# Optimization experiments

Measured on AMD Instinct MI355X. Metric: run time of the kernel, lower is better.

The kernel has to match this reference:

```python
import jax, jax.numpy as jnp
import numpy as np

B, S, D, H = 2, 1024, 1024, 16
HD = D // H
WINDOW = 256
FFN = 4 * D


def setup_inputs() -> dict:
    key = jax.random.key(0)
    ks = jax.random.split(key, 12)
    xav = lambda k, o, i: jax.random.normal(k, (o, i), jnp.float32) * np.sqrt(2.0 / (o + i))
    return {
        "x": jax.random.normal(ks[0], (B, S, D), jnp.float32),
        "wq": xav(ks[1], D, D), "bq": jnp.zeros((D,), jnp.float32),
        "wk": xav(ks[2], D, D), "bk": jnp.zeros((D,), jnp.float32),
        "wv": xav(ks[3], D, D), "bv": jnp.zeros((D,), jnp.float32),
        "wo": xav(ks[4], D, D), "bo": jnp.zeros((D,), jnp.float32),
        "attn_norm_w": jnp.ones((D,), jnp.float32),
        "ffn_norm_w": jnp.ones((D,), jnp.float32),
        "gate_w": xav(ks[5], FFN, D),
        "up_w": xav(ks[6], FFN, D),
        "down_w": xav(ks[7], D, FFN),
    }


def _rms(x, w):
    return x * jax.lax.rsqrt(jnp.mean(x * x, axis=-1, keepdims=True) + 1e-6) * w


def _rotate_half(x):
    x1, x2 = jnp.split(x, 2, axis=-1)
    return jnp.concatenate([-x2, x1], axis=-1)


def _rope_cos_sin(seq_len, head_dim):
    inv_freq = 1.0 / (10000.0 ** (jnp.arange(0, head_dim, 2, dtype=jnp.float32) / head_dim))
    freqs = jnp.arange(seq_len, dtype=jnp.float32)[:, None] * inv_freq[None, :]  # [S, HD/2]
    emb = jnp.concatenate([freqs, freqs], axis=-1)  # [S, HD]
    return jnp.cos(emb)[None, None], jnp.sin(emb)[None, None]  # [1,1,S,HD]


def reference(x, wq, bq, wk, bk, wv, bv, wo, bo, attn_norm_w, ffn_norm_w, gate_w, up_w, down_w):
    b, s, d = x.shape
    scale = 1.0 / np.sqrt(HD)
    residual = x
    h = _rms(x, attn_norm_w)
    q = (h @ wq.T + bq).reshape(b, s, H, HD).transpose(0, 2, 1, 3)  # [B,H,S,HD]
    k = (h @ wk.T + bk).reshape(b, s, H, HD).transpose(0, 2, 1, 3)
    v = (h @ wv.T + bv).reshape(b, s, H, HD).transpose(0, 2, 1, 3)
    cos, sin = _rope_cos_sin(s, HD)
    q = q * cos + _rotate_half(q) * sin
    k = k * cos + _rotate_half(k) * sin
    scores = jnp.einsum("bhqd,bhkd->bhqk", q, k) * scale  # dense [B,H,S,S]
    i = jnp.arange(s)[:, None]
    j = jnp.arange(s)[None, :]
    local_mask = (j <= i) & (i - j < WINDOW)  # causal sliding window
    scores = jnp.where(local_mask[None, None], scores, -jnp.inf)
    attn = jax.nn.softmax(scores, axis=-1)
    out = jnp.einsum("bhqk,bhkd->bhqd", attn, v)
    out = out.transpose(0, 2, 1, 3).reshape(b, s, d) @ wo.T + bo
    x = residual + out
    residual = x
    h = _rms(x, ffn_norm_w)
    ffn = (jax.nn.silu(h @ gate_w.T) * (h @ up_w.T)) @ down_w.T
    return (residual + ffn, attn)
```

## Files before the change

### kernel.cpp

```cpp
#include <hip/hip_runtime.h>

typedef unsigned short u16;
typedef unsigned int u32;
typedef __attribute__((ext_vector_type(8))) short short8;
typedef __attribute__((ext_vector_type(4))) float f32x4;

__device__ __forceinline__ float b2fu(u32 u) {
  union { u32 i; float f; } v; v.i = u << 16; return v.f;
}
__device__ __forceinline__ u16 f2bu(float f) {
  union { float f; u32 i; } v; v.f = f;
  u32 r = (v.i + 0x7fffu + ((v.i >> 16) & 1u)) >> 16;
  return (u16)r;
}
__device__ __forceinline__ void gl_lds16(const void* g, void* l) {
  __builtin_amdgcn_global_load_lds((const __attribute__((address_space(1))) void*)g,
                                   (__attribute__((address_space(3))) void*)l, 16, 0, 0);
}
__device__ __forceinline__ short8 ld_lds_b8(const u16* p) {
  uint2 a = *(const uint2*)p;
  uint2 b = *(const uint2*)(p + 4);
  union { u32 u[4]; short8 s; } v;
  v.u[0] = a.x; v.u[1] = a.y; v.u[2] = b.x; v.u[3] = b.y;
  return v.s;
}

__global__ __launch_bounds__(256) void cvt_front(
    const float* __restrict__ wq, const float* __restrict__ wk,
    const float* __restrict__ wv, const float* __restrict__ wo,
    const float* __restrict__ wg, const float* __restrict__ wu,
    const float* __restrict__ wd, u16* __restrict__ dst,
    const float* __restrict__ bq, const float* __restrict__ bk,
    const float* __restrict__ bv, float* __restrict__ bqkv,
    const float* __restrict__ x, const float* __restrict__ anw,
    u16* __restrict__ h1)
{
  __shared__ float red[4];
  if (blockIdx.x >= 16387) {
    const int row = blockIdx.x - 16387;
    const int t = threadIdx.x;
    float4 v = ((const float4*)(x + (size_t)row * 1024))[t];
    float ss = v.x * v.x + v.y * v.y + v.z * v.z + v.w * v.w;
#pragma unroll
    for (int m = 32; m > 0; m >>= 1) ss += __shfl_xor(ss, m, 64);
    if ((t & 63) == 0) red[t >> 6] = ss;
    __syncthreads();
    float tot = red[0] + red[1] + red[2] + red[3];
    float r = rsqrtf(tot * (1.0f / 1024.0f) + 1e-6f);
    float4 wv4 = ((const float4*)anw)[t];
    ushort4 o = make_ushort4(f2bu(v.x * r * wv4.x), f2bu(v.y * r * wv4.y),
                             f2bu(v.z * r * wv4.z), f2bu(v.w * r * wv4.w));
    ((ushort4*)(h1 + (size_t)row * 1024))[t] = o;
    return;
  }
  if (blockIdx.x >= 16384) {
    const int s = blockIdx.x - 16384;
    const float* bsrc = (s == 0) ? bq : (s == 1) ? bk : bv;
    const int o = threadIdx.x * 4;
    *(float4*)(bqkv + s * 1024 + o) = *(const float4*)(bsrc + o);
    return;
  }
  size_t e = ((size_t)blockIdx.x * 256 + threadIdx.x) * 4;
  size_t seg = e >> 20;
  const float* src; size_t soff;
  if      (seg == 0) { src = wq; soff = e; }
  else if (seg == 1) { src = wk; soff = e - ((size_t)1 << 20); }
  else if (seg == 2) { src = wv; soff = e - ((size_t)2 << 20); }
  else if (seg == 3) { src = wo; soff = e - ((size_t)3 << 20); }
  else if (seg < 12) {
    size_t idx = e - ((size_t)4 << 20);
    int rc = (int)(idx >> 10);
    int col = (int)(idx & 1023);
    int bi = rc >> 5, j = rc & 31;
    if (j < 16) { src = wg; soff = (size_t)(bi * 16 + j) * 1024 + col; }
    else        { src = wu; soff = (size_t)(bi * 16 + j - 16) * 1024 + col; }
  }
  else { src = wd; soff = e - ((size_t)12 << 20); }
  float4 v = *(const float4*)(src + soff);
  *(ushort4*)(dst + e) = make_ushort4(f2bu(v.x), f2bu(v.y), f2bu(v.z), f2bu(v.w));
}

__global__ __launch_bounds__(256) void rmsnorm_kernel(
    const float* __restrict__ x, const float* __restrict__ w, u16* __restrict__ out)
{
  const int row = blockIdx.x;
  const int t = threadIdx.x;
  float4 v = ((const float4*)(x + (size_t)row * 1024))[t];
  float ss = v.x * v.x + v.y * v.y + v.z * v.z + v.w * v.w;
#pragma unroll
  for (int m = 32; m > 0; m >>= 1) ss += __shfl_xor(ss, m, 64);
  __shared__ float red[4];
  if ((t & 63) == 0) red[t >> 6] = ss;
  __syncthreads();
  float tot = red[0] + red[1] + red[2] + red[3];
  float r = rsqrtf(tot * (1.0f / 1024.0f) + 1e-6f);
  float4 wv = ((const float4*)w)[t];
  ushort4 o = make_ushort4(f2bu(v.x * r * wv.x), f2bu(v.y * r * wv.y),
                           f2bu(v.z * r * wv.z), f2bu(v.w * r * wv.w));
  ((ushort4*)(out + (size_t)row * 1024))[t] = o;
}

template<int TMB, int TNB, int EPI, bool HAS_BIAS, bool HAS_RES, bool SPLIT>
__global__ __launch_bounds__(256) void gemm_bt(
    const u16* __restrict__ A, const u16* __restrict__ B, float* __restrict__ C,
    const float* __restrict__ bias, const float* __restrict__ res,
    int M, int N, int K, int lda,
    u16* __restrict__ P0, u16* __restrict__ P1, u16* __restrict__ P2)
{
  constexpr int BK = 32;
  constexpr int WTM = TMB / 2, WTN = TNB / 2;
  constexpr int MT = WTM / 16, NT = WTN / 16;
  __shared__ u16 As[TMB * BK];
  __shared__ u16 Bs[TNB * BK];
  const int t = threadIdx.x;
  const int w = t >> 6, l = t & 63;
  const int wm = (w >> 1) * WTM, wn = (w & 1) * WTN;
  const int lr = l & 15, lq = l >> 4;
  const int tile_m = blockIdx.y * TMB, tile_n = blockIdx.x * TNB;
  const int kb = SPLIT ? blockIdx.z * K : 0;
  if (SPLIT) C += (size_t)blockIdx.z * M * N;

  f32x4 acc[MT][NT] = {};

  const int sr = t >> 2;
  const int sc8 = (t & 3) * 8;
  const u16* Ab = A + (size_t)(tile_m + sr) * lda + kb + sc8;
  const u16* Bb = B + (size_t)(tile_n + sr) * lda + kb + sc8;

  for (int kk = 0; kk < K; kk += BK) {
#pragma unroll
    for (int i = 0; i < TMB / 64; ++i)
      gl_lds16(Ab + kk + (size_t)i * 64 * lda, &As[t * 8 + i * 2048]);
#pragma unroll
    for (int i = 0; i < TNB / 64; ++i)
      gl_lds16(Bb + kk + (size_t)i * 64 * lda, &Bs[t * 8 + i * 2048]);
    __syncthreads();
    short8 af[MT], bfr[NT];
#pragma unroll
    for (int mt = 0; mt < MT; ++mt)
      af[mt] = *(const short8*)&As[(wm + mt * 16 + lr) * BK + lq * 8];
#pragma unroll
    for (int nt = 0; nt < NT; ++nt)
      bfr[nt] = *(const short8*)&Bs[(wn + nt * 16 + lr) * BK + lq * 8];
#pragma unroll
    for (int mt = 0; mt < MT; ++mt)
#pragma unroll
      for (int nt = 0; nt < NT; ++nt)
        acc[mt][nt] = __builtin_amdgcn_mfma_f32_16x16x32_bf16(af[mt], bfr[nt], acc[mt][nt], 0, 0, 0);
    __syncthreads();
  }

  if (EPI == 0) {
#pragma unroll
    for (int nt = 0; nt < NT; ++nt) {
      const int col = tile_n + wn + nt * 16 + lr;
      const float bv = HAS_BIAS ? bias[col] : 0.0f;
#pragma unroll
      for (int mt = 0; mt < MT; ++mt) {
        const int row0 = tile_m + wm + mt * 16 + lq * 4;
#pragma unroll
        for (int r = 0; r < 4; ++r) {
          const size_t off = (size_t)(row0 + r) * N + col;
          float v = acc[mt][nt][r] + bv;
          if (HAS_RES) v += res[off];
          C[off] = v;
        }
      }
    }
  } else if (EPI == 1) {
    const int colbase = tile_n + wn;
    const int seg = colbase >> 10;
    const int h = (colbase >> 6) & 15;
    u16* dstb = (seg == 0) ? P0 : (seg == 1) ? P1 : P2;
    float bv[NT];
#pragma unroll
    for (int nt = 0; nt < NT; ++nt) bv[nt] = bias[colbase + nt * 16 + lr];
#pragma unroll
    for (int mt = 0; mt < MT; ++mt) {
      const int row0 = tile_m + wm + mt * 16 + lq * 4;
#pragma unroll
      for (int r = 0; r < 4; ++r) {
        const int row = row0 + r;
        const int s = row & 1023, b = row >> 10;
        u16* dst = dstb + (((size_t)(b * 16 + h) << 10) + s) * 64;
        if (seg < 2) {
#pragma unroll
          for (int np = 0; np < 2; ++np) {
            const int i = np * 16 + lr;
            const float th = (float)s * exp2f(-0.4152410118609203f * (float)i);
            float sn, cs; __sincosf(th, &sn, &cs);
            const float g0 = acc[mt][np][r] + bv[np];
            const float g2 = acc[mt][np + 2][r] + bv[np + 2];
            dst[i]      = f2bu(g0 * cs - g2 * sn);
            dst[i + 32] = f2bu(g2 * cs + g0 * sn);
          }
        } else {
#pragma unroll
          for (int nt = 0; nt < NT; ++nt)
            dst[nt * 16 + lr] = f2bu(acc[mt][nt][r] + bv[nt]);
        }
      }
    }
  } else {
#pragma unroll
    for (int nt = 0; nt < NT; nt += 2) {
      const int feat = (((tile_n + wn + nt * 16) >> 5) << 4) + lr;
#pragma unroll
      for (int mt = 0; mt < MT; ++mt) {
        const int row0 = tile_m + wm + mt * 16 + lq * 4;
#pragma unroll
        for (int r = 0; r < 4; ++r) {
          const float g = acc[mt][nt][r];
          const float u = acc[mt][nt + 1][r];
          const float a = g / (1.0f + __expf(-g)) * u;
          P0[(size_t)(row0 + r) * (N >> 1) + feat] = f2bu(a);
        }
      }
    }
  }
}

__global__ __launch_bounds__(256) void reduce2_kernel(
    const float* __restrict__ p, const float* __restrict__ bias,
    const float* __restrict__ res, float* __restrict__ out)
{
  const size_t i = ((size_t)blockIdx.x * 256 + threadIdx.x) * 4;
  float4 a = *(const float4*)(p + i);
  float4 b = *(const float4*)(p + i + 2097152);
  float4 r = *(const float4*)(res + i);
  float4 bv = *(const float4*)(bias + (i & 1023));
  float4 o;
  o.x = r.x + bv.x + a.x + b.x;
  o.y = r.y + bv.y + a.y + b.y;
  o.z = r.z + bv.z + a.z + b.z;
  o.w = r.w + bv.w + a.w + b.w;
  *(float4*)(out + i) = o;
}

__global__ __launch_bounds__(256) void reduce4_kernel(
    const float* __restrict__ p, const float* __restrict__ res, float* __restrict__ out)
{
  const size_t i = ((size_t)blockIdx.x * 256 + threadIdx.x) * 4;
  float4 a = *(const float4*)(p + i);
  float4 b = *(const float4*)(p + i + 2097152);
  float4 c = *(const float4*)(p + i + 2 * 2097152);
  float4 d = *(const float4*)(p + i + 3 * 2097152);
  float4 r = *(const float4*)(res + i);
  float4 o;
  o.x = r.x + a.x + b.x + c.x + d.x;
  o.y = r.y + a.y + b.y + c.y + d.y;
  o.z = r.z + a.z + b.z + c.z + d.z;
  o.w = r.w + a.w + b.w + c.w + d.w;
  *(float4*)(out + i) = o;
}

#define KP 68
#define PP 292

__global__ __launch_bounds__(256) void attn_kernel(
    const u16* __restrict__ qb, const u16* __restrict__ kb, const u16* __restrict__ vb,
    float* __restrict__ probs, u16* __restrict__ ctx)
{
  __shared__ u16 Kbuf[288 * KP];
  __shared__ u16 Vbuf[288 * KP];
  __shared__ float smax[2][32];
  __shared__ float ssum[2][32];
  u16* Pbuf = Kbuf;

  const int blk = blockIdx.x;
  const int qt = blk & 31, bh = blk >> 5;
  const int b = bh >> 4, h = bh & 15;
  const int q0 = qt << 5;
  const int kstart = (q0 > 255) ? (q0 - 255) : 0;
  const int span = q0 + 32 - kstart;
  const int t = threadIdx.x;
  const int w = t >> 6, l = t & 63;
  const int lr = l & 15, lq = l >> 4;
  const int mw = w & 1, nh = w >> 1;
  const size_t bhS = (size_t)bh << 10;

  {
    const u16* kg = kb + ((bhS + (size_t)kstart) << 6);
    const u16* vg = vb + ((bhS + (size_t)kstart) << 6);
    for (int idx = t; idx < 288 * 8; idx += 256) {
      const int r = idx >> 3, c = (idx & 7) << 3;
      uint4 kv4 = make_uint4(0, 0, 0, 0), vv4 = make_uint4(0, 0, 0, 0);
      if (r < span) {
        kv4 = *(const uint4*)&kg[(r << 6) + c];
        vv4 = *(const uint4*)&vg[(r << 6) + c];
      }
      *(uint2*)&Kbuf[r * KP + c]     = make_uint2(kv4.x, kv4.y);
      *(uint2*)&Kbuf[r * KP + c + 4] = make_uint2(kv4.z, kv4.w);
      *(uint2*)&Vbuf[r * KP + c]     = make_uint2(vv4.x, vv4.y);
      *(uint2*)&Vbuf[r * KP + c + 4] = make_uint2(vv4.z, vv4.w);
    }
  }
  short8 qa0, qa1;
  {
    const u16* qrow = qb + ((bhS + (size_t)(q0 + mw * 16 + lr)) << 6) + lq * 8;
    qa0 = *(const short8*)qrow;
    qa1 = *(const short8*)(qrow + 32);
  }
  __syncthreads();

  f32x4 acc[9];
#pragma unroll
  for (int i = 0; i < 9; ++i) acc[i] = (f32x4){0.f, 0.f, 0.f, 0.f};
#pragma unroll
  for (int i = 0; i < 9; ++i) {
    const int nt = nh + 2 * i;
    const u16* kr = &Kbuf[(nt * 16 + lr) * KP + lq * 8];
    short8 kf0 = ld_lds_b8(kr);
    short8 kf1 = ld_lds_b8(kr + 32);
    acc[i] = __builtin_amdgcn_mfma_f32_16x16x32_bf16(qa0, kf0, acc[i], 0, 0, 0);
    acc[i] = __builtin_amdgcn_mfma_f32_16x16x32_bf16(qa1, kf1, acc[i], 0, 0, 0);
  }

  const int rbase = mw * 16 + lq * 4;
  float rmax[4] = {-1e30f, -1e30f, -1e30f, -1e30f};
#pragma unroll
  for (int i = 0; i < 9; ++i) {
    const int jg = kstart + (nh + 2 * i) * 16 + lr;
#pragma unroll
    for (int r = 0; r < 4; ++r) {
      const int q = q0 + rbase + r;
      const bool valid = (jg >= q - 255) && (jg <= q);
      const float v = valid ? acc[i][r] * 0.125f : -1e30f;
      acc[i][r] = v;
      rmax[r] = fmaxf(rmax[r], v);
    }
  }
#pragma unroll
  for (int r = 0; r < 4; ++r) {
    float m_ = rmax[r];
    m_ = fmaxf(m_, __shfl_xor(m_, 1, 64));
    m_ = fmaxf(m_, __shfl_xor(m_, 2, 64));
    m_ = fmaxf(m_, __shfl_xor(m_, 4, 64));
    m_ = fmaxf(m_, __shfl_xor(m_, 8, 64));
    rmax[r] = m_;
  }
  if (lr == 0) {
#pragma unroll
    for (int r = 0; r < 4; ++r) smax[nh][rbase + r] = rmax[r];
  }
  __syncthreads();
#pragma unroll
  for (int r = 0; r < 4; ++r)
    rmax[r] = fmaxf(smax[0][rbase + r], smax[1][rbase + r]);
  float rsum[4] = {0.f, 0.f, 0.f, 0.f};
#pragma unroll
  for (int i = 0; i < 9; ++i)
#pragma unroll
    for (int r = 0; r < 4; ++r) {
      const float p = exp2f((acc[i][r] - rmax[r]) * 1.44269504f);
      acc[i][r] = p;
      rsum[r] += p;
    }
#pragma unroll
  for (int r = 0; r < 4; ++r) {
    float s_ = rsum[r];
    s_ += __shfl_xor(s_, 1, 64);
    s_ += __shfl_xor(s_, 2, 64);
    s_ += __shfl_xor(s_, 4, 64);
    s_ += __shfl_xor(s_, 8, 64);
    rsum[r] = s_;
  }
  if (lr == 0) {
#pragma unroll
    for (int r = 0; r < 4; ++r) ssum[nh][rbase + r] = rsum[r];
  }
  __syncthreads();

  float inv4[4];
#pragma unroll
  for (int r = 0; r < 4; ++r)
    inv4[r] = 1.0f / (ssum[0][rbase + r] + ssum[1][rbase + r]);
#pragma unroll
  for (int i = 0; i < 9; ++i) {
    const int nt = nh + 2 * i;
#pragma unroll
    for (int r = 0; r < 4; ++r)
      Pbuf[(rbase + r) * PP + nt * 16 + lr] = f2bu(acc[i][r] * inv4[r]);
  }
  __syncthreads();

  {
    const int row = t >> 3;
    const int q = q0 + row;
    const int c0 = (t & 7) << 7;
    const int lo = q - 255;
    float* prow = probs + ((bhS + (size_t)q) << 10) + c0;
    const u16* pr = &Pbuf[row * PP];
#pragma unroll 4
    for (int cc = 0; cc < 128; cc += 4) {
      const int c = c0 + cc;
      float4 o;
      o.x = (c + 0 >= lo && c + 0 <= q) ? b2fu(pr[c + 0 - kstart]) : 0.0f;
      o.y = (c + 1 >= lo && c + 1 <= q) ? b2fu(pr[c + 1 - kstart]) : 0.0f;
      o.z = (c + 2 >= lo && c + 2 <= q) ? b2fu(pr[c + 2 - kstart]) : 0.0f;
      o.w = (c + 3 >= lo && c + 3 <= q) ? b2fu(pr[c + 3 - kstart]) : 0.0f;
      *(float4*)&prow[cc] = o;
    }
  }

  const int n0 = (w >> 1) * 2;
  f32x4 oacc[2] = {};
#pragma unroll
  for (int ks = 0; ks < 9; ++ks) {
    short8 pa = ld_lds_b8(&Pbuf[(mw * 16 + lr) * PP + ks * 32 + lq * 8]);
#pragma unroll
    for (int nn = 0; nn < 2; ++nn) {
      const int d = (n0 + nn) * 16 + lr;
      union { u16 u[8]; short8 s; } bf_;
#pragma unroll
      for (int jj = 0; jj < 8; ++jj)
        bf_.u[jj] = Vbuf[(ks * 32 + lq * 8 + jj) * KP + d];
      oacc[nn] = __builtin_amdgcn_mfma_f32_16x16x32_bf16(pa, bf_.s, oacc[nn], 0, 0, 0);
    }
  }
#pragma unroll
  for (int nn = 0; nn < 2; ++nn) {
    const int d = (n0 + nn) * 16 + lr;
#pragma unroll
    for (int r = 0; r < 4; ++r) {
      const int q = q0 + rbase + r;
      ctx[(((size_t)(b * 1024 + q)) << 10) + (h << 6) + d] = f2bu(oacc[nn][r]);
    }
  }
}

extern "C" void kernel_launch(void* const* d_in, const int* in_sizes, int n_in,
                              void* d_out, int out_size, void* d_ws, size_t ws_size,
                              hipStream_t stream) {
  (void)in_sizes; (void)n_in; (void)out_size; (void)ws_size;
  const float* x   = (const float*)d_in[0];
  const float* wq  = (const float*)d_in[1];
  const float* bq  = (const float*)d_in[2];
  const float* wk  = (const float*)d_in[3];
  const float* bk  = (const float*)d_in[4];
  const float* wv  = (const float*)d_in[5];
  const float* bv  = (const float*)d_in[6];
  const float* wo  = (const float*)d_in[7];
  const float* bo  = (const float*)d_in[8];
  const float* anw = (const float*)d_in[9];
  const float* fnw = (const float*)d_in[10];
  const float* wg  = (const float*)d_in[11];
  const float* wu  = (const float*)d_in[12];
  const float* wd  = (const float*)d_in[13];

  char* ws = (char*)d_ws;
  u16*   wbf  = (u16*)ws;
  float* bqkv = (float*)(ws + ((size_t)32 << 20));
  u16*   h1   = (u16*)(ws + ((size_t)32 << 20) + (16 << 10));
  char*  R    = ws + ((size_t)36 << 20) + (16 << 10);
  u16*   qbp  = (u16*)R;
  u16*   kbp  = (u16*)(R + ((size_t)4 << 20));
  u16*   vbp  = (u16*)(R + ((size_t)8 << 20));
  u16*   ctx  = (u16*)(R + ((size_t)12 << 20));
  float* x1   = (float*)(R + ((size_t)16 << 20));
  u16*   h2   = (u16*)(R + ((size_t)24 << 20));
  u16*   act  = (u16*)(R + ((size_t)28 << 20));
  float* pbuf = (float*)(R + ((size_t)44 << 20));
  float* pbuf2= (float*)(R + ((size_t)76 << 20));

  float* out0  = (float*)d_out;
  float* probs = (float*)d_out + 2097152;

  cvt_front<<<18435, 256, 0, stream>>>(wq, wk, wv, wo, wg, wu, wd, wbf,
                                       bq, bk, bv, bqkv, x, anw, h1);

  gemm_bt<128, 128, 1, true, false, false><<<dim3(24, 16), 256, 0, stream>>>(
      h1, wbf, nullptr, bqkv, nullptr, 2048, 3072, 1024, 1024, qbp, kbp, vbp);
  attn_kernel<<<1024, 256, 0, stream>>>(qbp, kbp, vbp, probs, ctx);
  gemm_bt<64, 128, 0, false, false, true><<<dim3(8, 32, 2), 256, 0, stream>>>(
      ctx, wbf + ((size_t)3 << 20), pbuf2, nullptr, nullptr, 2048, 1024, 512, 1024,
      nullptr, nullptr, nullptr);
  reduce2_kernel<<<2048, 256, 0, stream>>>(pbuf2, bo, x, x1);

  rmsnorm_kernel<<<2048, 256, 0, stream>>>(x1, fnw, h2);
  gemm_bt<128, 128, 2, false, false, false><<<dim3(64, 16), 256, 0, stream>>>(
      h2, wbf + ((size_t)4 << 20), nullptr, nullptr, nullptr, 2048, 8192, 1024, 1024,
      act, nullptr, nullptr);
  gemm_bt<64, 128, 0, false, false, true><<<dim3(8, 32, 4), 256, 0, stream>>>(
      act, wbf + ((size_t)12 << 20), pbuf, nullptr, nullptr, 2048, 1024, 1024, 4096,
      nullptr, nullptr, nullptr);
  reduce4_kernel<<<2048, 256, 0, stream>>>(pbuf, x1, out0);
}
```

Measured before the change: 432.3 us.

## Fuse out-projection split-K reduction into GEMM epilogue and stage attention output through LDS

```diff
diff --git a/kernel.cpp b/kernel.cpp
--- a/kernel.cpp
+++ b/kernel.cpp
@@ -220,23 +220,6 @@
   }
 }
 
-__global__ __launch_bounds__(256) void reduce2_kernel(
-    const float* __restrict__ p, const float* __restrict__ bias,
-    const float* __restrict__ res, float* __restrict__ out)
-{
-  const size_t i = ((size_t)blockIdx.x * 256 + threadIdx.x) * 4;
-  float4 a = *(const float4*)(p + i);
-  float4 b = *(const float4*)(p + i + 2097152);
-  float4 r = *(const float4*)(res + i);
-  float4 bv = *(const float4*)(bias + (i & 1023));
-  float4 o;
-  o.x = r.x + bv.x + a.x + b.x;
-  o.y = r.y + bv.y + a.y + b.y;
-  o.z = r.z + bv.z + a.z + b.z;
-  o.w = r.w + bv.w + a.w + b.w;
-  *(float4*)(out + i) = o;
-}
-
 __global__ __launch_bounds__(256) void reduce4_kernel(
     const float* __restrict__ p, const float* __restrict__ res, float* __restrict__ out)
 {
@@ -418,14 +401,23 @@
       oacc[nn] = __builtin_amdgcn_mfma_f32_16x16x32_bf16(pa, bf_.s, oacc[nn], 0, 0, 0);
     }
   }
+  __syncthreads();
 #pragma unroll
   for (int nn = 0; nn < 2; ++nn) {
     const int d = (n0 + nn) * 16 + lr;
 #pragma unroll
-    for (int r = 0; r < 4; ++r) {
-      const int q = q0 + rbase + r;
-      ctx[(((size_t)(b * 1024 + q)) << 10) + (h << 6) + d] = f2bu(oacc[nn][r]);
-    }
+    for (int r = 0; r < 4; ++r)
+      Vbuf[(rbase + r) * KP + d] = f2bu(oacc[nn][r]);
+  }
+  __syncthreads();
+  {
+    const int row = t >> 3, c = (t & 7) * 8;
+    const u16* sr_ = &Vbuf[row * KP + c];
+    uint2 a0 = *(const uint2*)sr_;
+    uint2 a1 = *(const uint2*)(sr_ + 4);
+    u16* cr = ctx + (((size_t)(b * 1024 + q0 + row)) << 10) + (h << 6) + c;
+    union { uint2 a[2]; uint4 q4; } u_; u_.a[0] = a0; u_.a[1] = a1;
+    *(uint4*)cr = u_.q4;
   }
 }
 
@@ -461,7 +453,6 @@
   u16*   h2   = (u16*)(R + ((size_t)24 << 20));
   u16*   act  = (u16*)(R + ((size_t)28 << 20));
   float* pbuf = (float*)(R + ((size_t)44 << 20));
-  float* pbuf2= (float*)(R + ((size_t)76 << 20));
 
   float* out0  = (float*)d_out;
   float* probs = (float*)d_out + 2097152;
@@ -469,13 +460,12 @@
   cvt_front<<<18435, 256, 0, stream>>>(wq, wk, wv, wo, wg, wu, wd, wbf,
                                        bq, bk, bv, bqkv, x, anw, h1);
 
-  gemm_bt<128, 128, 1, true, false, false><<<dim3(24, 16), 256, 0, stream>>>(
+  gemm_bt<64, 128, 1, true, false, false><<<dim3(24, 32), 256, 0, stream>>>(
       h1, wbf, nullptr, bqkv, nullptr, 2048, 3072, 1024, 1024, qbp, kbp, vbp);
   attn_kernel<<<1024, 256, 0, stream>>>(qbp, kbp, vbp, probs, ctx);
-  gemm_bt<64, 128, 0, false, false, true><<<dim3(8, 32, 2), 256, 0, stream>>>(
-      ctx, wbf + ((size_t)3 << 20), pbuf2, nullptr, nullptr, 2048, 1024, 512, 1024,
+  gemm_bt<64, 128, 0, true, true, false><<<dim3(8, 32), 256, 0, stream>>>(
+      ctx, wbf + ((size_t)3 << 20), x1, bo, x, 2048, 1024, 1024, 1024,
       nullptr, nullptr, nullptr);
-  reduce2_kernel<<<2048, 256, 0, stream>>>(pbuf2, bo, x, x1);
 
   rmsnorm_kernel<<<2048, 256, 0, stream>>>(x1, fnw, h2);
   gemm_bt<128, 128, 2, false, false, false><<<dim3(64, 16), 256, 0, stream>>>(
```

Result: no change. 425.9 us (-1.5%).
